# Kernel tuning notes

Measured on AMD Instinct MI355X. Metric: run time of the kernel, lower is better.

Reference implementation:

```python
import jax, jax.numpy as jnp
import numpy as np

B, DX, DY, K, H = 131072, 256, 32, 4, 128
TIMESTEPS = 1000
LR, REG, SW = 0.1, 0.01, 1.0


def setup_inputs() -> dict:
    key = jax.random.key(0)
    ks = jax.random.split(key, 12)
    n = lambda k, shp, s=0.05: (jax.random.normal(k, shp) * s).astype(jnp.float32)
    return {
        "x": jax.random.normal(ks[0], (B, DX), jnp.float32),
        "t": jax.random.randint(ks[1], (B,), 0, K),
        "e_w1": n(ks[2], (DX + DY, H)), "e_b1": jnp.zeros((H,), jnp.float32),
        "e_w2": n(ks[3], (H, H)),       "e_b2": jnp.zeros((H,), jnp.float32),
        "e_w3": n(ks[4], (H, K)),       "e_b3": jnp.zeros((K,), jnp.float32),
        "s_xw": n(ks[5], (DX, H)),      "s_xb": jnp.zeros((H,), jnp.float32),
        "s_yw": n(ks[6], (DY, H)),      "s_yb": jnp.zeros((H,), jnp.float32),
        "s_temb": n(ks[7], (K, H)),
        "s_t1w": n(ks[8], (1, H)),      "s_t1b": jnp.zeros((H,), jnp.float32),
        "s_t2w": n(ks[9], (H, H)),      "s_t2b": jnp.zeros((H,), jnp.float32),
        "tr1w": n(ks[10], (4 * H, H)),  "tr1b": jnp.zeros((H,), jnp.float32),
        "tr2w": n(ks[11], (H, K)),      "tr2b": jnp.zeros((K,), jnp.float32),
        "steps": 20,
    }


def reference(x, t, e_w1, e_b1, e_w2, e_b2, e_w3, e_b3,
              s_xw, s_xb, s_yw, s_yb, s_temb, s_t1w, s_t1b, s_t2w, s_t2b,
              tr1w, tr1b, tr2w, tr2b, steps):
    tc = jnp.maximum(t, 0)                      # clamp_min(0)
    tci = tc[:, None]                           # [B,1] gather index
    valid = (t >= 0).astype(jnp.float32)[:, None]
    tau = jnp.maximum(tc.astype(jnp.float32) / TIMESTEPS, 1e-6)[:, None]  # [B,1]

    # y-independent precomputations (hoisted out of the loop)
    hx_e = x @ e_w1[:DX] + e_b1                 # energy first layer, x part [B,H]
    hx_s = x @ s_xw + s_xb                      # score x_proj [B,H]
    temb = s_temb[tc]                           # t embedding [B,H]
    th = jax.nn.silu(tau @ s_t1w + s_t1b) @ s_t2w + s_t2b  # time_fc [B,H]

    def total_fn(y):
        # EnergyNet: Linear-ReLU-Linear-ReLU-Linear on cat([x,y])
        h1 = jax.nn.relu(hx_e + y @ e_w1[DX:])
        e_all = jax.nn.relu(h1 @ e_w2 + e_b2) @ e_w3 + e_b3          # [B,K]
        e = jnp.take_along_axis(e_all, tci, axis=1)                  # [B,1]
        tot = e + REG * jnp.sum(y * y, axis=1, keepdims=True)
        # ScoreNet trunk on cat([x_proj, y_proj, t_embed, time_fc])
        hy = y @ s_yw + s_yb
        h = jnp.concatenate([hx_s, hy, temb, th], axis=-1)           # [B,4H]
        logits = jax.nn.silu(h @ tr1w + tr1b) @ tr2w + tr2b          # [B,K]
        ce = jax.nn.logsumexp(logits, axis=-1, keepdims=True) - jnp.take_along_axis(logits, tci, axis=1)
        return jnp.sum(tot + SW * ce * valid)

    grad_fn = jax.grad(total_fn)

    def step(carry, _):
        y, done = carry
        g = grad_fn(y)
        done = done | (jnp.sqrt(jnp.sum(g * g)) < 1e-3)  # torch: break before update
        y = jnp.where(done, y, y - LR * g)
        return (y, done), None

    y0 = jnp.zeros((x.shape[0], DY), jnp.float32)
    (y, _), _ = jax.lax.scan(step, (y0, jnp.array(False)), None, length=steps)
    return y
```

## Files before the change

### kernel.cpp

```cpp
#include <hip/hip_runtime.h>
#include <hip/hip_bf16.h>

#define DXc 256
#define DYc 32
#define Kc 4
#define Hc 128
#define LRf 0.1f
#define REGf 0.01f
#define TSTEPS 1000

typedef __attribute__((ext_vector_type(8))) short s8b;
typedef __attribute__((ext_vector_type(4))) float f32x4;

#define MFMA16(a, b, c) __builtin_amdgcn_mfma_f32_16x16x32_bf16((a), (b), (c), 0, 0, 0)

#define MFMA6(A0, A1, A2, B0, B1, B2, acc)      \
    do {                                        \
        acc = MFMA16((A0), (B0), acc);          \
        acc = MFMA16((A0), (B1), acc);          \
        acc = MFMA16((A1), (B0), acc);          \
        acc = MFMA16((A0), (B2), acc);          \
        acc = MFMA16((A1), (B1), acc);          \
        acc = MFMA16((A2), (B0), acc);          \
    } while (0)

__device__ __forceinline__ float hipart(float a) {
    return __uint_as_float(__float_as_uint(a) & 0xffff0000u);
}
__device__ __forceinline__ unsigned hi2(float a, float b) {
    return (__float_as_uint(a) >> 16) | (__float_as_uint(b) & 0xffff0000u);
}
__device__ __forceinline__ void wsplit(float x, unsigned short* __restrict__ h,
                                       unsigned short* __restrict__ l) {
    unsigned u = __float_as_uint(x);
    *h = (unsigned short)(u >> 16);
    float hf = __uint_as_float(u & 0xffff0000u);
    *l = (unsigned short)(__float_as_uint(x - hf) >> 16);
}
__device__ __forceinline__ void wsplit3(float x, unsigned short* __restrict__ p0,
                                        unsigned short* __restrict__ p1,
                                        unsigned short* __restrict__ p2) {
    unsigned u = __float_as_uint(x);
    *p0 = (unsigned short)(u >> 16);
    float r1 = x - __uint_as_float(u & 0xffff0000u);
    unsigned u1 = __float_as_uint(r1);
    *p1 = (unsigned short)(u1 >> 16);
    float r2 = r1 - __uint_as_float(u1 & 0xffff0000u);
    *p2 = (unsigned short)(__float_as_uint(r2) >> 16);
}
__device__ __forceinline__ void split3x8(const float* v, s8b& A0, s8b& A1, s8b& A2) {
    union { s8b s; unsigned u[4]; } P0, P1, P2;
    #pragma unroll
    for (int m = 0; m < 4; ++m) {
        float a = v[2 * m], b = v[2 * m + 1];
        unsigned ua = __float_as_uint(a), ub = __float_as_uint(b);
        P0.u[m] = (ua >> 16) | (ub & 0xffff0000u);
        float ra = a - __uint_as_float(ua & 0xffff0000u);
        float rb = b - __uint_as_float(ub & 0xffff0000u);
        unsigned ura = __float_as_uint(ra), urb = __float_as_uint(rb);
        P1.u[m] = (ura >> 16) | (urb & 0xffff0000u);
        float ra2 = ra - __uint_as_float(ura & 0xffff0000u);
        float rb2 = rb - __uint_as_float(urb & 0xffff0000u);
        P2.u[m] = (__float_as_uint(ra2) >> 16) | (__float_as_uint(rb2) & 0xffff0000u);
    }
    A0 = P0.s; A1 = P1.s; A2 = P2.s;
}
__device__ __forceinline__ void split3pack4(const float* v, uint2& Q0, uint2& Q1, uint2& Q2) {
    float r1[4], r2[4];
    #pragma unroll
    for (int i = 0; i < 4; ++i) {
        r1[i] = v[i] - hipart(v[i]);
        r2[i] = r1[i] - hipart(r1[i]);
    }
    Q0.x = hi2(v[0], v[1]);   Q0.y = hi2(v[2], v[3]);
    Q1.x = hi2(r1[0], r1[1]); Q1.y = hi2(r1[2], r1[3]);
    Q2.x = hi2(r2[0], r2[1]); Q2.y = hi2(r2[2], r2[3]);
}
__device__ __forceinline__ void split2pack4(const float* v, uint2& Q0, uint2& Q1) {
    Q0.x = hi2(v[0], v[1]); Q0.y = hi2(v[2], v[3]);
    float r0 = v[0] - hipart(v[0]), r1 = v[1] - hipart(v[1]);
    float r2 = v[2] - hipart(v[2]), r3 = v[3] - hipart(v[3]);
    Q1.x = hi2(r0, r1); Q1.y = hi2(r2, r3);
}

__global__ __launch_bounds__(256) void setup_kernel(
    const float* __restrict__ e_w1, const float* __restrict__ s_xw,
    const float* __restrict__ s_yw, const float* __restrict__ s_temb,
    const float* __restrict__ s_t1w, const float* __restrict__ s_t1b,
    const float* __restrict__ s_t2w, const float* __restrict__ s_t2b,
    const float* __restrict__ tr1w, const float* __restrict__ tr1b,
    const float* __restrict__ s_xb, const float* __restrict__ s_yb,
    const float* __restrict__ e_w2, float* __restrict__ d0,
    unsigned short* __restrict__ WcatTb0, unsigned short* __restrict__ WcatTb1,
    unsigned short* __restrict__ WcatTb2,
    unsigned short* __restrict__ W1Tb0, unsigned short* __restrict__ W1Tb1,
    unsigned short* __restrict__ W1Tb2,
    unsigned short* __restrict__ ew2Tb0, unsigned short* __restrict__ ew2Tb1,
    unsigned short* __restrict__ ew2Tb2,
    unsigned short* __restrict__ ew2bh, unsigned short* __restrict__ ew2bl,
    unsigned short* __restrict__ Wdybh, unsigned short* __restrict__ Wdybl)
{
    const int b = blockIdx.x;
    const int t = threadIdx.x;
    if (b < 64) {
        #pragma unroll
        for (int i = 0; i < 2; ++i) {
            int idx = t + 256 * i;
            int k = 4 * b + (idx >> 7);
            int c = idx & 127;
            float acc = 0.f;
            for (int h = 0; h < 128; ++h)
                acc += s_xw[k * 128 + h] * tr1w[h * 128 + c];
            wsplit3(acc, &WcatTb0[(128 + c) * 256 + k], &WcatTb1[(128 + c) * 256 + k],
                    &WcatTb2[(128 + c) * 256 + k]);
            float ev = e_w1[k * 128 + c];
            wsplit3(ev, &WcatTb0[c * 256 + k], &WcatTb1[c * 256 + k],
                    &WcatTb2[c * 256 + k]);
        }
    } else if (b == 64) {
        #pragma unroll
        for (int i = 0; i < 16; ++i) {
            int idx = t + 256 * i;
            int d = idx >> 7, c = idx & 127;
            float acc = 0.f;
            for (int h = 0; h < 128; ++h)
                acc += s_yw[d * 128 + h] * tr1w[(128 + h) * 128 + c];
            wsplit3(acc, &W1Tb0[(128 + c) * 32 + d], &W1Tb1[(128 + c) * 32 + d],
                    &W1Tb2[(128 + c) * 32 + d]);
            wsplit(acc, &Wdybh[d * 256 + c], &Wdybl[d * 256 + c]);
        }
    } else if (b == 65) {
        #pragma unroll
        for (int i = 0; i < 16; ++i) {
            int idx = t + 256 * i;
            int d = idx >> 7, c = idx & 127;
            float v = e_w1[(DXc + d) * 128 + c];
            wsplit3(v, &W1Tb0[c * 32 + d], &W1Tb1[c * 32 + d], &W1Tb2[c * 32 + d]);
            wsplit(v, &Wdybh[d * 256 + 128 + c], &Wdybl[d * 256 + 128 + c]);
        }
    } else if (b == 66) {
        #pragma unroll
        for (int i = 0; i < 64; ++i) {
            int idx = t + 256 * i;
            int h = idx >> 7, c = idx & 127;
            float v = e_w2[h * 128 + c];
            wsplit3(v, &ew2Tb0[c * 128 + h], &ew2Tb1[c * 128 + h],
                    &ew2Tb2[c * 128 + h]);
            wsplit(v, &ew2bh[h * 128 + c], &ew2bl[h * 128 + c]);
        }
    } else {
        __shared__ float thS[4][128];
        #pragma unroll
        for (int i = 0; i < 2; ++i) {
            int idx = t + 256 * i;
            int tt = idx >> 7, c = idx & 127;
            float tau = (float)tt / (float)TSTEPS;
            if (tau < 1e-6f) tau = 1e-6f;
            float acc = s_t2b[c];
            for (int h = 0; h < 128; ++h) {
                float aa = tau * s_t1w[h] + s_t1b[h];
                float s = 1.f / (1.f + expf(-aa));
                acc += aa * s * s_t2w[h * 128 + c];
            }
            thS[tt][c] = acc;
        }
        __syncthreads();
        #pragma unroll
        for (int i = 0; i < 2; ++i) {
            int idx = t + 256 * i;
            int tt = idx >> 7, c = idx & 127;
            float acc = tr1b[c];
            for (int h = 0; h < 128; ++h) {
                acc += s_temb[tt * 128 + h] * tr1w[(256 + h) * 128 + c];
                acc += thS[tt][h]           * tr1w[(384 + h) * 128 + c];
                acc += s_yb[h]              * tr1w[(128 + h) * 128 + c];
                acc += s_xb[h]              * tr1w[h * 128 + c];
            }
            d0[tt * 128 + c] = acc;
        }
    }
}

__global__ __launch_bounds__(256) void rowpre_kernel(
    const float* __restrict__ x, const int* __restrict__ tin,
    const unsigned short* __restrict__ WcatTb0,
    const unsigned short* __restrict__ WcatTb1,
    const unsigned short* __restrict__ WcatTb2,
    const float* __restrict__ e_b1, const float* __restrict__ d0,
    float* __restrict__ hxeP, float* __restrict__ cbP)
{
    __shared__ int tS[64];
    const int t = threadIdx.x;
    const int r0 = blockIdx.x * 64;
    const int w = t >> 6;
    const int l = t & 63;
    const int g = l >> 4, q = l & 15;
    if (t < 64) { int tv = tin[r0 + t]; tS[t] = tv > 0 ? tv : 0; }
    __syncthreads();

    for (int st = 0; st < 4; ++st) {
        const int smp = r0 + st * 16 + q;
        s8b Xb0[8], Xb1[8], Xb2[8];
        #pragma unroll
        for (int kc = 0; kc < 8; ++kc) {
            const float* xp = &x[(size_t)smp * 256 + kc * 32 + g * 8];
            float4 xa = *(const float4*)xp;
            float4 xb = *(const float4*)(xp + 4);
            float xv[8] = {xa.x, xa.y, xa.z, xa.w, xb.x, xb.y, xb.z, xb.w};
            split3x8(xv, Xb0[kc], Xb1[kc], Xb2[kc]);
        }
        #pragma unroll
        for (int ci = 0; ci < 4; ++ci) {
            const int colt = w * 4 + ci;
            f32x4 acc = {0.f, 0.f, 0.f, 0.f};
            #pragma unroll
            for (int kc = 0; kc < 8; ++kc) {
                const int wo = (colt * 16 + q) * 256 + kc * 32 + g * 8;
                s8b A0 = *(const s8b*)&WcatTb0[wo];
                s8b A1 = *(const s8b*)&WcatTb1[wo];
                s8b A2 = *(const s8b*)&WcatTb2[wo];
                MFMA6(A0, A1, A2, Xb0[kc], Xb1[kc], Xb2[kc], acc);
            }
            const int cb = colt * 16 + g * 4;
            if (colt < 8) {
                float4 bv = *(const float4*)&e_b1[cb];
                float4 o = {acc[0] + bv.x, acc[1] + bv.y, acc[2] + bv.z, acc[3] + bv.w};
                *(float4*)&hxeP[(size_t)smp * 128 + cb] = o;
            } else {
                const int cc = cb - 128;
                float4 dd = *(const float4*)&d0[tS[st * 16 + q] * 128 + cc];
                float4 o = {acc[0] + dd.x, acc[1] + dd.y, acc[2] + dd.z, acc[3] + dd.w};
                *(float4*)&cbP[(size_t)smp * 128 + cc] = o;
            }
        }
    }
}

__global__ __launch_bounds__(512) void iterate_kernel(
    const float* __restrict__ hxeP, const float* __restrict__ cbP,
    const unsigned short* __restrict__ W1Tb0, const unsigned short* __restrict__ W1Tb1,
    const unsigned short* __restrict__ W1Tb2,
    const unsigned short* __restrict__ ew2Tb0, const unsigned short* __restrict__ ew2Tb1,
    const unsigned short* __restrict__ ew2Tb2,
    const unsigned short* __restrict__ ew2bh, const unsigned short* __restrict__ ew2bl,
    const unsigned short* __restrict__ Wdybh, const unsigned short* __restrict__ Wdybl,
    const float* __restrict__ e_w3, const float* __restrict__ tr2w,
    const float* __restrict__ tr2b, const float* __restrict__ e_b2,
    const int* __restrict__ tin, const int* __restrict__ stepsPtr,
    float* __restrict__ yout)
{
    __shared__ __align__(16) unsigned short H1a[32 * 136];
    __shared__ __align__(16) unsigned short H1b[32 * 136];
    __shared__ __align__(16) unsigned short H1c[32 * 136];
    __shared__ __align__(16) unsigned short DAa[32 * 136], DAb[32 * 136];
    __shared__ __align__(16) float U[32 * 140];
    __shared__ __align__(16) float yS[32 * 36];
    __shared__ float ew3S[512];
    __shared__ float eb2S[128];
    __shared__ float vSs[32];
    __shared__ int tcS[32];

    const int t = threadIdx.x;
    const int r0 = blockIdx.x * 32;
    const int w = t >> 6;
    const int l = t & 63;
    const int g = l >> 4;
    const int q = l & 15;
    const int row = t >> 4;
    const int p = t & 15;
    const int hA = 4 * p;
    const int hB = 64 + 4 * p;

    if (t < 32) {
        int tv = tin[r0 + t];
        tcS[t] = tv > 0 ? tv : 0;
        vSs[t] = (tv >= 0) ? 1.f : 0.f;
    }
    if (t < 128) eb2S[t] = e_b2[t];
    ew3S[t] = e_w3[t];
    for (int i = t; i < 32 * 36; i += 512) yS[i] = 0.f;

    float4 trw4[8];
    #pragma unroll
    for (int j = 0; j < 4; ++j) {
        trw4[j]     = *(const float4*)&tr2w[(hA + j) * 4];
        trw4[4 + j] = *(const float4*)&tr2w[(hB + j) * 4];
    }
    s8b W1A0[2], W1A1[2], W1A2[2];
    #pragma unroll
    for (int ci = 0; ci < 2; ++ci) {
        const int arow = (2 * w + ci) * 16 + q;
        W1A0[ci] = *(const s8b*)&W1Tb0[arow * 32 + g * 8];
        W1A1[ci] = *(const s8b*)&W1Tb1[arow * 32 + g * 8];
        W1A2[ci] = *(const s8b*)&W1Tb2[arow * 32 + g * 8];
    }
    const float tb0 = tr2b[0], tb1 = tr2b[1], tb2 = tr2b[2], tb3 = tr2b[3];
    const int nsteps = stepsPtr[0];

    __syncthreads();

    for (int step = 0; step < nsteps; ++step) {
        #pragma unroll
        for (int ct = 0; ct < 2; ++ct) {
            float4 ya = *(const float4*)&yS[(ct * 16 + q) * 36 + g * 8];
            float4 yb = *(const float4*)&yS[(ct * 16 + q) * 36 + g * 8 + 4];
            float yv[8] = {ya.x, ya.y, ya.z, ya.w, yb.x, yb.y, yb.z, yb.w};
            s8b Y0, Y1, Y2;
            split3x8(yv, Y0, Y1, Y2);
            #pragma unroll
            for (int ci = 0; ci < 2; ++ci) {
                const int colt = 2 * w + ci;
                f32x4 acc = {0.f, 0.f, 0.f, 0.f};
                MFMA6(W1A0[ci], W1A1[ci], W1A2[ci], Y0, Y1, Y2, acc);
                if (w < 4) {
                    const float4 vb = *(const float4*)
                        &hxeP[(size_t)(r0 + ct * 16 + q) * 128 + colt * 16 + g * 4];
                    float v[4];
                    v[0] = acc[0] + vb.x; v[1] = acc[1] + vb.y;
                    v[2] = acc[2] + vb.z; v[3] = acc[3] + vb.w;
                    #pragma unroll
                    for (int j = 0; j < 4; ++j) v[j] = v[j] > 0.f ? v[j] : 0.f;
                    uint2 Q0, Q1, Q2;
                    split3pack4(v, Q0, Q1, Q2);
                    const int off = (ct * 16 + q) * 136 + colt * 16 + g * 4;
                    *(uint2*)&H1a[off] = Q0;
                    *(uint2*)&H1b[off] = Q1;
                    *(uint2*)&H1c[off] = Q2;
                } else {
                    const int cc = (colt - 8) * 16 + g * 4;
                    const float4 vb = *(const float4*)
                        &cbP[(size_t)(r0 + ct * 16 + q) * 128 + cc];
                    float4 o = {acc[0] + vb.x, acc[1] + vb.y,
                                acc[2] + vb.z, acc[3] + vb.w};
                    *(float4*)&U[(ct * 16 + q) * 140 + cc] = o;
                }
            }
        }
        __syncthreads();

        {
            float aval[8], sval[8];
            float lg0 = 0.f, lg1 = 0.f, lg2 = 0.f, lg3 = 0.f;
            float4 v0 = *(const float4*)&U[row * 140 + hA];
            float4 v1 = *(const float4*)&U[row * 140 + hB];
            aval[0] = v0.x; aval[1] = v0.y; aval[2] = v0.z; aval[3] = v0.w;
            aval[4] = v1.x; aval[5] = v1.y; aval[6] = v1.z; aval[7] = v1.w;
            #pragma unroll
            for (int j = 0; j < 8; ++j) {
                float a = aval[j];
                float s = 1.f / (1.f + __expf(-a));
                sval[j] = s;
                float u = a * s;
                lg0 += u * trw4[j].x; lg1 += u * trw4[j].y;
                lg2 += u * trw4[j].z; lg3 += u * trw4[j].w;
            }
            #pragma unroll
            for (int m = 1; m < 16; m <<= 1) {
                lg0 += __shfl_xor(lg0, m);
                lg1 += __shfl_xor(lg1, m);
                lg2 += __shfl_xor(lg2, m);
                lg3 += __shfl_xor(lg3, m);
            }
            lg0 += tb0; lg1 += tb1; lg2 += tb2; lg3 += tb3;
            float mx = fmaxf(fmaxf(lg0, lg1), fmaxf(lg2, lg3));
            float e0 = __expf(lg0 - mx), e1 = __expf(lg1 - mx);
            float e2 = __expf(lg2 - mx), e3 = __expf(lg3 - mx);
            float inv = 1.f / (e0 + e1 + e2 + e3);
            int tcr = tcS[row];
            float vd = vSs[row];
            float dl0 = (e0 * inv - (tcr == 0 ? 1.f : 0.f)) * vd;
            float dl1 = (e1 * inv - (tcr == 1 ? 1.f : 0.f)) * vd;
            float dl2 = (e2 * inv - (tcr == 2 ? 1.f : 0.f)) * vd;
            float dl3 = (e3 * inv - (tcr == 3 ? 1.f : 0.f)) * vd;
            #pragma unroll
            for (int j = 0; j < 8; ++j) {
                float a = aval[j], s = sval[j];
                float du = dl0 * trw4[j].x + dl1 * trw4[j].y
                         + dl2 * trw4[j].z + dl3 * trw4[j].w;
                aval[j] = du * s * (1.f + a * (1.f - s));
            }
            float rl[8];
            #pragma unroll
            for (int j = 0; j < 8; ++j) rl[j] = aval[j] - hipart(aval[j]);
            uint2 QhA = {hi2(aval[0], aval[1]), hi2(aval[2], aval[3])};
            uint2 QhB = {hi2(aval[4], aval[5]), hi2(aval[6], aval[7])};
            uint2 QlA = {hi2(rl[0], rl[1]), hi2(rl[2], rl[3])};
            uint2 QlB = {hi2(rl[4], rl[5]), hi2(rl[6], rl[7])};
            *(uint2*)&DAa[row * 136 + hA] = QhA;
            *(uint2*)&DAa[row * 136 + hB] = QhB;
            *(uint2*)&DAb[row * 136 + hA] = QlA;
            *(uint2*)&DAb[row * 136 + hB] = QlB;
        }
        __syncthreads();

        {
            unsigned short* DZh = (unsigned short*)U;
            unsigned short* DZl = DZh + 32 * 136;
            f32x4 acc0 = {0.f, 0.f, 0.f, 0.f};
            f32x4 acc1 = {0.f, 0.f, 0.f, 0.f};
            #pragma unroll
            for (int kc = 0; kc < 4; ++kc) {
                const int b0 = q * 136 + kc * 32 + g * 8;
                const int b1 = (16 + q) * 136 + kc * 32 + g * 8;
                s8b B0a = *(const s8b*)&H1a[b0];
                s8b B0b = *(const s8b*)&H1b[b0];
                s8b B0c = *(const s8b*)&H1c[b0];
                s8b B1a = *(const s8b*)&H1a[b1];
                s8b B1b = *(const s8b*)&H1b[b1];
                s8b B1c = *(const s8b*)&H1c[b1];
                const int wo = (w * 16 + q) * 128 + kc * 32 + g * 8;
                s8b A0 = *(const s8b*)&ew2Tb0[wo];
                s8b A1 = *(const s8b*)&ew2Tb1[wo];
                s8b A2 = *(const s8b*)&ew2Tb2[wo];
                MFMA6(A0, A1, A2, B0a, B0b, B0c, acc0);
                MFMA6(A0, A1, A2, B1a, B1b, B1c, acc1);
            }
            const int cb = w * 16 + g * 4;
            const float4 eb = *(const float4*)&eb2S[cb];
            {
                const int smp = q;
                const int tcr = tcS[smp];
                float dz[4];
                dz[0] = (acc0[0] + eb.x) > 0.f ? ew3S[(cb + 0) * 4 + tcr] : 0.f;
                dz[1] = (acc0[1] + eb.y) > 0.f ? ew3S[(cb + 1) * 4 + tcr] : 0.f;
                dz[2] = (acc0[2] + eb.z) > 0.f ? ew3S[(cb + 2) * 4 + tcr] : 0.f;
                dz[3] = (acc0[3] + eb.w) > 0.f ? ew3S[(cb + 3) * 4 + tcr] : 0.f;
                uint2 Q0, Q1;
                split2pack4(dz, Q0, Q1);
                *(uint2*)&DZh[smp * 136 + cb] = Q0;
                *(uint2*)&DZl[smp * 136 + cb] = Q1;
            }
            {
                const int smp = 16 + q;
                const int tcr = tcS[smp];
                float dz[4];
                dz[0] = (acc1[0] + eb.x) > 0.f ? ew3S[(cb + 0) * 4 + tcr] : 0.f;
                dz[1] = (acc1[1] + eb.y) > 0.f ? ew3S[(cb + 1) * 4 + tcr] : 0.f;
                dz[2] = (acc1[2] + eb.z) > 0.f ? ew3S[(cb + 2) * 4 + tcr] : 0.f;
                dz[3] = (acc1[3] + eb.w) > 0.f ? ew3S[(cb + 3) * 4 + tcr] : 0.f;
                uint2 Q0, Q1;
                split2pack4(dz, Q0, Q1);
                *(uint2*)&DZh[smp * 136 + cb] = Q0;
                *(uint2*)&DZl[smp * 136 + cb] = Q1;
            }
        }
        __syncthreads();

        {
            const unsigned short* DZh = (const unsigned short*)U;
            const unsigned short* DZl = DZh + 32 * 136;
            f32x4 acc0 = {0.f, 0.f, 0.f, 0.f};
            f32x4 acc1 = {0.f, 0.f, 0.f, 0.f};
            #pragma unroll
            for (int kc = 0; kc < 4; ++kc) {
                const int b0 = q * 136 + kc * 32 + g * 8;
                const int b1 = (16 + q) * 136 + kc * 32 + g * 8;
                s8b B0h = *(const s8b*)&DZh[b0];
                s8b B0l = *(const s8b*)&DZl[b0];
                s8b B1h = *(const s8b*)&DZh[b1];
                s8b B1l = *(const s8b*)&DZl[b1];
                const int wo = (w * 16 + q) * 128 + kc * 32 + g * 8;
                s8b Ah = *(const s8b*)&ew2bh[wo];
                s8b Al = *(const s8b*)&ew2bl[wo];
                acc0 = MFMA16(Ah, B0h, acc0);
                acc0 = MFMA16(Al, B0h, acc0);
                acc0 = MFMA16(Ah, B0l, acc0);
                acc1 = MFMA16(Ah, B1h, acc1);
                acc1 = MFMA16(Al, B1h, acc1);
                acc1 = MFMA16(Ah, B1l, acc1);
            }
            const int hb = w * 16 + g * 4;
            {
                const int off = q * 136 + hb;
                const uint2 mh = *(const uint2*)&H1a[off];
                float v[4];
                v[0] = ((short)(mh.x & 0xffffu) > 0) ? acc0[0] : 0.f;
                v[1] = ((short)(mh.x >> 16)     > 0) ? acc0[1] : 0.f;
                v[2] = ((short)(mh.y & 0xffffu) > 0) ? acc0[2] : 0.f;
                v[3] = ((short)(mh.y >> 16)     > 0) ? acc0[3] : 0.f;
                uint2 Q0, Q1;
                split2pack4(v, Q0, Q1);
                *(uint2*)&H1a[off] = Q0;
                *(uint2*)&H1b[off] = Q1;
            }
            {
                const int off = (16 + q) * 136 + hb;
                const uint2 mh = *(const uint2*)&H1a[off];
                float v[4];
                v[0] = ((short)(mh.x & 0xffffu) > 0) ? acc1[0] : 0.f;
                v[1] = ((short)(mh.x >> 16)     > 0) ? acc1[1] : 0.f;
                v[2] = ((short)(mh.y & 0xffffu) > 0) ? acc1[2] : 0.f;
                v[3] = ((short)(mh.y >> 16)     > 0) ? acc1[3] : 0.f;
                uint2 Q0, Q1;
                split2pack4(v, Q0, Q1);
                *(uint2*)&H1a[off] = Q0;
                *(uint2*)&H1b[off] = Q1;
            }
        }
        __syncthreads();

        if (w < 4) {
            const int dt = w >> 1, st = w & 1;
            f32x4 acc = {0.f, 0.f, 0.f, 0.f};
            #pragma unroll
            for (int kc = 0; kc < 8; ++kc) {
                const int boff = (st * 16 + q) * 136 + (kc & 3) * 32 + g * 8;
                s8b bh, bl;
                if (kc < 4) { bh = *(const s8b*)&DAa[boff]; bl = *(const s8b*)&DAb[boff]; }
                else        { bh = *(const s8b*)&H1a[boff]; bl = *(const s8b*)&H1b[boff]; }
                const int aoff = (dt * 16 + q) * 256 + kc * 32 + g * 8;
                s8b ah = *(const s8b*)&Wdybh[aoff];
                s8b al = *(const s8b*)&Wdybl[aoff];
                acc = MFMA16(ah, bh, acc);
                acc = MFMA16(al, bh, acc);
                acc = MFMA16(ah, bl, acc);
            }
            const int smp = st * 16 + q;
            const int db = dt * 16 + g * 4;
            float4 yv4 = *(const float4*)&yS[smp * 36 + db];
            yv4.x -= LRf * (acc[0] + 2.f * REGf * yv4.x);
            yv4.y -= LRf * (acc[1] + 2.f * REGf * yv4.y);
            yv4.z -= LRf * (acc[2] + 2.f * REGf * yv4.z);
            yv4.w -= LRf * (acc[3] + 2.f * REGf * yv4.w);
            *(float4*)&yS[smp * 36 + db] = yv4;
        }
        __syncthreads();
    }

    {
        const int orow = t >> 4;
        const int d2 = (t & 15) * 2;
        *(float2*)&yout[(size_t)(r0 + orow) * 32 + d2] =
            *(const float2*)&yS[orow * 36 + d2];
    }
}

extern "C" void kernel_launch(void* const* d_in, const int* in_sizes, int n_in,
                              void* d_out, int out_size, void* d_ws, size_t ws_size,
                              hipStream_t stream)
{
    const float* x      = (const float*)d_in[0];
    const int*   tin    = (const int*)d_in[1];
    const float* e_w1   = (const float*)d_in[2];
    const float* e_b1   = (const float*)d_in[3];
    const float* e_w2   = (const float*)d_in[4];
    const float* e_b2   = (const float*)d_in[5];
    const float* e_w3   = (const float*)d_in[6];
    const float* s_xw   = (const float*)d_in[8];
    const float* s_xb   = (const float*)d_in[9];
    const float* s_yw   = (const float*)d_in[10];
    const float* s_yb   = (const float*)d_in[11];
    const float* s_temb = (const float*)d_in[12];
    const float* s_t1w  = (const float*)d_in[13];
    const float* s_t1b  = (const float*)d_in[14];
    const float* s_t2w  = (const float*)d_in[15];
    const float* s_t2b  = (const float*)d_in[16];
    const float* tr1w   = (const float*)d_in[17];
    const float* tr1b   = (const float*)d_in[18];
    const float* tr2w   = (const float*)d_in[19];
    const float* tr2b   = (const float*)d_in[20];
    const int*   steps  = (const int*)d_in[21];

    const int B = in_sizes[0] / DXc;

    float* ws   = (float*)d_ws;
    float* hxeP = ws;
    float* cbP  = hxeP + (size_t)B * 128;
    float* d0   = cbP  + (size_t)B * 128;

    unsigned short* W1Tb0   = (unsigned short*)(d0 + 4 * 128);
    unsigned short* W1Tb1   = W1Tb0   + 256 * 32;
    unsigned short* W1Tb2   = W1Tb1   + 256 * 32;
    unsigned short* ew2Tb0  = W1Tb2   + 256 * 32;
    unsigned short* ew2Tb1  = ew2Tb0  + 128 * 128;
    unsigned short* ew2Tb2  = ew2Tb1  + 128 * 128;
    unsigned short* ew2bh   = ew2Tb2  + 128 * 128;
    unsigned short* ew2bl   = ew2bh   + 128 * 128;
    unsigned short* Wdybh   = ew2bl   + 128 * 128;
    unsigned short* Wdybl   = Wdybh   + 32 * 256;
    unsigned short* WcatTb0 = Wdybl   + 32 * 256;
    unsigned short* WcatTb1 = WcatTb0 + 256 * 256;
    unsigned short* WcatTb2 = WcatTb1 + 256 * 256;

    setup_kernel<<<68, 256, 0, stream>>>(e_w1, s_xw, s_yw, s_temb, s_t1w, s_t1b,
                                         s_t2w, s_t2b, tr1w, tr1b, s_xb, s_yb,
                                         e_w2, d0,
                                         WcatTb0, WcatTb1, WcatTb2,
                                         W1Tb0, W1Tb1, W1Tb2,
                                         ew2Tb0, ew2Tb1, ew2Tb2,
                                         ew2bh, ew2bl, Wdybh, Wdybl);
    rowpre_kernel<<<B / 64, 256, 0, stream>>>(x, tin, WcatTb0, WcatTb1, WcatTb2,
                                              e_b1, d0, hxeP, cbP);
    iterate_kernel<<<B / 32, 512, 0, stream>>>(hxeP, cbP,
                                               W1Tb0, W1Tb1, W1Tb2,
                                               ew2Tb0, ew2Tb1, ew2Tb2,
                                               ew2bh, ew2bl, Wdybh, Wdybl,
                                               e_w3, tr2w, tr2b, e_b2, tin,
                                               steps, (float*)d_out);
}
```

Baseline: 2.816 ms.

## Reload W1 fragments per step, swap MFMA tile assignment, transpose e_w3 in LDS

W1 A-fragments are no longer held in registers for the whole step loop; they are reloaded from global memory at the start of each step to lower register pressure. In the two 128x128 layer-2 GEMMs, each wave now owns one 16-sample half and two output-column tiles, so the wave loads the LDS B fragments once and reads two weight tiles, where before it read both sample halves. e_w3 is stored transposed in shared memory so the dz gather becomes a single float4 read indexed by class. The cost is extra global and L2 weight traffic every step.

Result: slower. 3.339 ms (+18.5%).

```diff
diff --git a/kernel.cpp b/kernel.cpp
--- a/kernel.cpp
+++ b/kernel.cpp
@@ -255,7 +255,7 @@
     __shared__ __align__(16) unsigned short DAa[32 * 136], DAb[32 * 136];
     __shared__ __align__(16) float U[32 * 140];
     __shared__ __align__(16) float yS[32 * 36];
-    __shared__ float ew3S[512];
+    __shared__ float ew3TS[512];
     __shared__ float eb2S[128];
     __shared__ float vSs[32];
     __shared__ int tcS[32];
@@ -277,7 +277,10 @@
         vSs[t] = (tv >= 0) ? 1.f : 0.f;
     }
     if (t < 128) eb2S[t] = e_b2[t];
-    ew3S[t] = e_w3[t];
+    {
+        const int k = t >> 7, c = t & 127;
+        ew3TS[k * 128 + c] = e_w3[c * 4 + k];
+    }
     for (int i = t; i < 32 * 36; i += 512) yS[i] = 0.f;
 
     float4 trw4[8];
@@ -286,53 +289,55 @@
         trw4[j]     = *(const float4*)&tr2w[(hA + j) * 4];
         trw4[4 + j] = *(const float4*)&tr2w[(hB + j) * 4];
     }
-    s8b W1A0[2], W1A1[2], W1A2[2];
-    #pragma unroll
-    for (int ci = 0; ci < 2; ++ci) {
-        const int arow = (2 * w + ci) * 16 + q;
-        W1A0[ci] = *(const s8b*)&W1Tb0[arow * 32 + g * 8];
-        W1A1[ci] = *(const s8b*)&W1Tb1[arow * 32 + g * 8];
-        W1A2[ci] = *(const s8b*)&W1Tb2[arow * 32 + g * 8];
-    }
     const float tb0 = tr2b[0], tb1 = tr2b[1], tb2 = tr2b[2], tb3 = tr2b[3];
     const int nsteps = stepsPtr[0];
 
     __syncthreads();
 
     for (int step = 0; step < nsteps; ++step) {
-        #pragma unroll
-        for (int ct = 0; ct < 2; ++ct) {
-            float4 ya = *(const float4*)&yS[(ct * 16 + q) * 36 + g * 8];
-            float4 yb = *(const float4*)&yS[(ct * 16 + q) * 36 + g * 8 + 4];
-            float yv[8] = {ya.x, ya.y, ya.z, ya.w, yb.x, yb.y, yb.z, yb.w};
-            s8b Y0, Y1, Y2;
-            split3x8(yv, Y0, Y1, Y2);
+        {
+            s8b WA0[2], WA1[2], WA2[2];
             #pragma unroll
             for (int ci = 0; ci < 2; ++ci) {
-                const int colt = 2 * w + ci;
-                f32x4 acc = {0.f, 0.f, 0.f, 0.f};
-                MFMA6(W1A0[ci], W1A1[ci], W1A2[ci], Y0, Y1, Y2, acc);
-                if (w < 4) {
-                    const float4 vb = *(const float4*)
-                        &hxeP[(size_t)(r0 + ct * 16 + q) * 128 + colt * 16 + g * 4];
-                    float v[4];
-                    v[0] = acc[0] + vb.x; v[1] = acc[1] + vb.y;
-                    v[2] = acc[2] + vb.z; v[3] = acc[3] + vb.w;
-                    #pragma unroll
-                    for (int j = 0; j < 4; ++j) v[j] = v[j] > 0.f ? v[j] : 0.f;
-                    uint2 Q0, Q1, Q2;
-                    split3pack4(v, Q0, Q1, Q2);
-                    const int off = (ct * 16 + q) * 136 + colt * 16 + g * 4;
-                    *(uint2*)&H1a[off] = Q0;
-                    *(uint2*)&H1b[off] = Q1;
-                    *(uint2*)&H1c[off] = Q2;
-                } else {
-                    const int cc = (colt - 8) * 16 + g * 4;
-                    const float4 vb = *(const float4*)
-                        &cbP[(size_t)(r0 + ct * 16 + q) * 128 + cc];
-                    float4 o = {acc[0] + vb.x, acc[1] + vb.y,
-                                acc[2] + vb.z, acc[3] + vb.w};
-                    *(float4*)&U[(ct * 16 + q) * 140 + cc] = o;
+                const int arow = (2 * w + ci) * 16 + q;
+                WA0[ci] = *(const s8b*)&W1Tb0[arow * 32 + g * 8];
+                WA1[ci] = *(const s8b*)&W1Tb1[arow * 32 + g * 8];
+                WA2[ci] = *(const s8b*)&W1Tb2[arow * 32 + g * 8];
+            }
+            #pragma unroll
+            for (int ct = 0; ct < 2; ++ct) {
+                float4 ya = *(const float4*)&yS[(ct * 16 + q) * 36 + g * 8];
+                float4 yb = *(const float4*)&yS[(ct * 16 + q) * 36 + g * 8 + 4];
+                float yv[8] = {ya.x, ya.y, ya.z, ya.w, yb.x, yb.y, yb.z, yb.w};
+                s8b Y0, Y1, Y2;
+                split3x8(yv, Y0, Y1, Y2);
+                #pragma unroll
+                for (int ci = 0; ci < 2; ++ci) {
+                    const int colt = 2 * w + ci;
+                    f32x4 acc = {0.f, 0.f, 0.f, 0.f};
+                    MFMA6(WA0[ci], WA1[ci], WA2[ci], Y0, Y1, Y2, acc);
+                    if (w < 4) {
+                        const float4 vb = *(const float4*)
+                            &hxeP[(size_t)(r0 + ct * 16 + q) * 128 + colt * 16 + g * 4];
+                        float v[4];
+                        v[0] = acc[0] + vb.x; v[1] = acc[1] + vb.y;
+                        v[2] = acc[2] + vb.z; v[3] = acc[3] + vb.w;
+                        #pragma unroll
+                        for (int j = 0; j < 4; ++j) v[j] = v[j] > 0.f ? v[j] : 0.f;
+                        uint2 Q0, Q1, Q2;
+                        split3pack4(v, Q0, Q1, Q2);
+                        const int off = (ct * 16 + q) * 136 + colt * 16 + g * 4;
+                        *(uint2*)&H1a[off] = Q0;
+                        *(uint2*)&H1b[off] = Q1;
+                        *(uint2*)&H1c[off] = Q2;
+                    } else {
+                        const int cc = (colt - 8) * 16 + g * 4;
+                        const float4 vb = *(const float4*)
+                            &cbP[(size_t)(r0 + ct * 16 + q) * 128 + cc];
+                        float4 o = {acc[0] + vb.x, acc[1] + vb.y,
+                                    acc[2] + vb.z, acc[3] + vb.w};
+                        *(float4*)&U[(ct * 16 + q) * 140 + cc] = o;
+                    }
                 }
             }
         }
@@ -396,101 +401,85 @@
         {
             unsigned short* DZh = (unsigned short*)U;
             unsigned short* DZl = DZh + 32 * 136;
+            const int hf = w & 1;
+            const int ct0 = (w >> 1) * 2;
             f32x4 acc0 = {0.f, 0.f, 0.f, 0.f};
             f32x4 acc1 = {0.f, 0.f, 0.f, 0.f};
             #pragma unroll
             for (int kc = 0; kc < 4; ++kc) {
-                const int b0 = q * 136 + kc * 32 + g * 8;
-                const int b1 = (16 + q) * 136 + kc * 32 + g * 8;
-                s8b B0a = *(const s8b*)&H1a[b0];
-                s8b B0b = *(const s8b*)&H1b[b0];
-                s8b B0c = *(const s8b*)&H1c[b0];
-                s8b B1a = *(const s8b*)&H1a[b1];
-                s8b B1b = *(const s8b*)&H1b[b1];
-                s8b B1c = *(const s8b*)&H1c[b1];
-                const int wo = (w * 16 + q) * 128 + kc * 32 + g * 8;
-                s8b A0 = *(const s8b*)&ew2Tb0[wo];
-                s8b A1 = *(const s8b*)&ew2Tb1[wo];
-                s8b A2 = *(const s8b*)&ew2Tb2[wo];
-                MFMA6(A0, A1, A2, B0a, B0b, B0c, acc0);
-                MFMA6(A0, A1, A2, B1a, B1b, B1c, acc1);
-            }
-            const int cb = w * 16 + g * 4;
-            const float4 eb = *(const float4*)&eb2S[cb];
-            {
-                const int smp = q;
-                const int tcr = tcS[smp];
+                const int boff = (hf * 16 + q) * 136 + kc * 32 + g * 8;
+                s8b Ba = *(const s8b*)&H1a[boff];
+                s8b Bb = *(const s8b*)&H1b[boff];
+                s8b Bc = *(const s8b*)&H1c[boff];
+                const int wo0 = ((ct0 + 0) * 16 + q) * 128 + kc * 32 + g * 8;
+                const int wo1 = ((ct0 + 1) * 16 + q) * 128 + kc * 32 + g * 8;
+                s8b A00 = *(const s8b*)&ew2Tb0[wo0];
+                s8b A01 = *(const s8b*)&ew2Tb1[wo0];
+                s8b A02 = *(const s8b*)&ew2Tb2[wo0];
+                MFMA6(A00, A01, A02, Ba, Bb, Bc, acc0);
+                s8b A10 = *(const s8b*)&ew2Tb0[wo1];
+                s8b A11 = *(const s8b*)&ew2Tb1[wo1];
+                s8b A12 = *(const s8b*)&ew2Tb2[wo1];
+                MFMA6(A10, A11, A12, Ba, Bb, Bc, acc1);
+            }
+            const int smp = hf * 16 + q;
+            const int tcr = tcS[smp];
+            #pragma unroll
+            for (int c2 = 0; c2 < 2; ++c2) {
+                const f32x4& acc = c2 ? acc1 : acc0;
+                const int cb = (ct0 + c2) * 16 + g * 4;
+                const float4 eb = *(const float4*)&eb2S[cb];
+                const float4 g4 = *(const float4*)&ew3TS[tcr * 128 + cb];
                 float dz[4];
-                dz[0] = (acc0[0] + eb.x) > 0.f ? ew3S[(cb + 0) * 4 + tcr] : 0.f;
-                dz[1] = (acc0[1] + eb.y) > 0.f ? ew3S[(cb + 1) * 4 + tcr] : 0.f;
-                dz[2] = (acc0[2] + eb.z) > 0.f ? ew3S[(cb + 2) * 4 + tcr] : 0.f;
-                dz[3] = (acc0[3] + eb.w) > 0.f ? ew3S[(cb + 3) * 4 + tcr] : 0.f;
+                dz[0] = (acc[0] + eb.x) > 0.f ? g4.x : 0.f;
+                dz[1] = (acc[1] + eb.y) > 0.f ? g4.y : 0.f;
+                dz[2] = (acc[2] + eb.z) > 0.f ? g4.z : 0.f;
+                dz[3] = (acc[3] + eb.w) > 0.f ? g4.w : 0.f;
                 uint2 Q0, Q1;
                 split2pack4(dz, Q0, Q1);
                 *(uint2*)&DZh[smp * 136 + cb] = Q0;
                 *(uint2*)&DZl[smp * 136 + cb] = Q1;
             }
-            {
-                const int smp = 16 + q;
-                const int tcr = tcS[smp];
-                float dz[4];
-                dz[0] = (acc1[0] + eb.x) > 0.f ? ew3S[(cb + 0) * 4 + tcr] : 0.f;
-                dz[1] = (acc1[1] + eb.y) > 0.f ? ew3S[(cb + 1) * 4 + tcr] : 0.f;
-                dz[2] = (acc1[2] + eb.z) > 0.f ? ew3S[(cb + 2) * 4 + tcr] : 0.f;
-                dz[3] = (acc1[3] + eb.w) > 0.f ? ew3S[(cb + 3) * 4 + tcr] : 0.f;
-                uint2 Q0, Q1;
-                split2pack4(dz, Q0, Q1);
-                *(uint2*)&DZh[smp * 136 + cb] = Q0;
-                *(uint2*)&DZl[smp * 136 + cb] = Q1;
-            }
         }
         __syncthreads();
 
         {
             const unsigned short* DZh = (const unsigned short*)U;
             const unsigned short* DZl = DZh + 32 * 136;
+            const int hf = w & 1;
+            const int ht0 = (w >> 1) * 2;
             f32x4 acc0 = {0.f, 0.f, 0.f, 0.f};
             f32x4 acc1 = {0.f, 0.f, 0.f, 0.f};
             #pragma unroll
             for (int kc = 0; kc < 4; ++kc) {
-                const int b0 = q * 136 + kc * 32 + g * 8;
-                const int b1 = (16 + q) * 136 + kc * 32 + g * 8;
-                s8b B0h = *(const s8b*)&DZh[b0];
-                s8b B0l = *(const s8b*)&DZl[b0];
-                s8b B1h = *(const s8b*)&DZh[b1];
-                s8b B1l = *(const s8b*)&DZl[b1];
-                const int wo = (w * 16 + q) * 128 + kc * 32 + g * 8;
-                s8b Ah = *(const s8b*)&ew2bh[wo];
-                s8b Al = *(const s8b*)&ew2bl[wo];
-                acc0 = MFMA16(Ah, B0h, acc0);
-                acc0 = MFMA16(Al, B0h, acc0);
-                acc0 = MFMA16(Ah, B0l, acc0);
-                acc1 = MFMA16(Ah, B1h, acc1);
-                acc1 = MFMA16(Al, B1h, acc1);
-                acc1 = MFMA16(Ah, B1l, acc1);
-            }
-            const int hb = w * 16 + g * 4;
-            {
-                const int off = q * 136 + hb;
+                const int boff = (hf * 16 + q) * 136 + kc * 32 + g * 8;
+                s8b Bh = *(const s8b*)&DZh[boff];
+                s8b Bl = *(const s8b*)&DZl[boff];
+                const int wo0 = ((ht0 + 0) * 16 + q) * 128 + kc * 32 + g * 8;
+                const int wo1 = ((ht0 + 1) * 16 + q) * 128 + kc * 32 + g * 8;
+                s8b A0h = *(const s8b*)&ew2bh[wo0];
+                s8b A0l = *(const s8b*)&ew2bl[wo0];
+                acc0 = MFMA16(A0h, Bh, acc0);
+                acc0 = MFMA16(A0l, Bh, acc0);
+                acc0 = MFMA16(A0h, Bl, acc0);
+                s8b A1h = *(const s8b*)&ew2bh[wo1];
+                s8b A1l = *(const s8b*)&ew2bl[wo1];
+                acc1 = MFMA16(A1h, Bh, acc1);
+                acc1 = MFMA16(A1l, Bh, acc1);
+                acc1 = MFMA16(A1h, Bl, acc1);
+            }
+            const int smp = hf * 16 + q;
+            #pragma unroll
+            for (int c2 = 0; c2 < 2; ++c2) {
+                const f32x4& acc = c2 ? acc1 : acc0;
+                const int hb = (ht0 + c2) * 16 + g * 4;
+                const int off = smp * 136 + hb;
                 const uint2 mh = *(const uint2*)&H1a[off];
                 float v[4];
-                v[0] = ((short)(mh.x & 0xffffu) > 0) ? acc0[0] : 0.f;
-                v[1] = ((short)(mh.x >> 16)     > 0) ? acc0[1] : 0.f;
-                v[2] = ((short)(mh.y & 0xffffu) > 0) ? acc0[2] : 0.f;
-                v[3] = ((short)(mh.y >> 16)     > 0) ? acc0[3] : 0.f;
-                uint2 Q0, Q1;
-                split2pack4(v, Q0, Q1);
-                *(uint2*)&H1a[off] = Q0;
-                *(uint2*)&H1b[off] = Q1;
-            }
-            {
-                const int off = (16 + q) * 136 + hb;
-                const uint2 mh = *(const uint2*)&H1a[off];
-                float v[4];
-                v[0] = ((short)(mh.x & 0xffffu) > 0) ? acc1[0] : 0.f;
-                v[1] = ((short)(mh.x >> 16)     > 0) ? acc1[1] : 0.f;
-                v[2] = ((short)(mh.y & 0xffffu) > 0) ? acc1[2] : 0.f;
-                v[3] = ((short)(mh.y >> 16)     > 0) ? acc1[3] : 0.f;
+                v[0] = ((short)(mh.x & 0xffffu) > 0) ? acc[0] : 0.f;
+                v[1] = ((short)(mh.x >> 16)     > 0) ? acc[1] : 0.f;
+                v[2] = ((short)(mh.y & 0xffffu) > 0) ? acc[2] : 0.f;
+                v[3] = ((short)(mh.y >> 16)     > 0) ? acc[3] : 0.f;
                 uint2 Q0, Q1;
                 split2pack4(v, Q0, Q1);
                 *(uint2*)&H1a[off] = Q0;
```
